# Performance work log

Hardware: AMD Instinct MI355X
Metric: run time of the kernel (lower is better)

Reference implementation:

```python
import jax, jax.numpy as jnp
import numpy as np

N, D = 512, 64          # n_objects, object_dim
HG, OG = 256, 256       # g hidden, g output
HF, OF = 256, 64        # f hidden, f output


def setup_inputs() -> dict:
    key = jax.random.key(0)
    ks = jax.random.split(key, 16)
    s = 0.05
    inp = {
        "x": jax.random.normal(ks[0], (N, D), dtype=jnp.float32),
        "q": jax.random.normal(ks[1], (D,), dtype=jnp.float32),
        # MLP g: input 3*D -> HG -> OG (ReLU after every layer, nonlinear=True)
        "g_w1": jax.random.normal(ks[2], (3 * D, HG), dtype=jnp.float32) * s,
        "g_b1": jnp.zeros((HG,), dtype=jnp.float32),
        "g_w2": jax.random.normal(ks[3], (HG, OG), dtype=jnp.float32) * s,
        "g_b2": jnp.zeros((OG,), dtype=jnp.float32),
        # query_expand: D -> HG -> OG (nonlinear=True)
        "qe_w1": jax.random.normal(ks[4], (D, HG), dtype=jnp.float32) * s,
        "qe_b1": jnp.zeros((HG,), dtype=jnp.float32),
        "qe_w2": jax.random.normal(ks[5], (HG, OG), dtype=jnp.float32) * s,
        "qe_b2": jnp.zeros((OG,), dtype=jnp.float32),
        # MLP f: OG -> HF -> OF (ReLU on hidden only, nonlinear=False)
        "f_w1": jax.random.normal(ks[6], (OG, HF), dtype=jnp.float32) * s,
        "f_b1": jnp.zeros((HF,), dtype=jnp.float32),
        "f_w2": jax.random.normal(ks[7], (HF, OF), dtype=jnp.float32) * s,
        "f_b2": jnp.zeros((OF,), dtype=jnp.float32),
    }
    return inp


def reference(x, q, g_w1, g_b1, g_w2, g_b2, qe_w1, qe_b1, qe_w2, qe_b2,
              f_w1, f_b1, f_w2, f_b2):
    n, d = x.shape
    # pair (a,b): first half x_i = x[b], second half x_j = x[a], then query q
    xi = jnp.broadcast_to(x[None, :, :], (n, n, d))   # repeats x along dim 0
    xj = jnp.broadcast_to(x[:, None, :], (n, n, d))   # repeats x along dim 1
    qb = jnp.broadcast_to(q[None, None, :], (n, n, d))
    pair_concat = jnp.concatenate([xi, xj, qb], axis=-1).reshape(n * n, 3 * d)
    # g MLP (ReLU after every layer since nonlinear=True)
    h = jax.nn.relu(pair_concat @ g_w1 + g_b1)
    relations = jax.nn.relu(h @ g_w2 + g_b2)          # [N*N, OG]
    # attentional weighting
    qh = jax.nn.relu(q @ qe_w1 + qe_b1)
    q_exp = jax.nn.relu(qh @ qe_w2 + qe_b2)           # [OG]
    c = jax.nn.softmax(relations @ q_exp, axis=0)     # [N*N]
    embedding = jnp.sum(relations * c[:, None], axis=0)  # [OG]
    # f MLP (no final nonlinearity)
    fh = jax.nn.relu(embedding @ f_w1 + f_b1)
    out = fh @ f_w2 + f_b2                            # [OF]
    return out
```

## Files before the change

### kernel.cpp

```cpp
#include <hip/hip_runtime.h>
#include <hip/hip_bf16.h>

typedef __attribute__((ext_vector_type(8))) short s16x8;
typedef __attribute__((ext_vector_type(4))) float f32x4;

#define NSLOT 128

__device__ __forceinline__ short f2bf(float f) {
    union { float f; unsigned u; } c; c.f = f;
    unsigned u = c.u;
    return (short)((u + 0x7fffu + ((u >> 16) & 1u)) >> 16);
}
__device__ __forceinline__ float bf2f(short s) {
    union { unsigned u; float f; } c;
    c.u = ((unsigned)(unsigned short)s) << 16;
    return c.f;
}
__device__ __forceinline__ unsigned pk2(float lo, float hi) {
    __hip_bfloat162 p = __float22bfloat162_rn(make_float2(lo, hi));
    return *reinterpret_cast<unsigned*>(&p);
}

#define GLD16(gp, lp) __builtin_amdgcn_global_load_lds( \
    (const __attribute__((address_space(1))) unsigned int*)(gp), \
    (__attribute__((address_space(3))) unsigned int*)(lp), 16, 0, 0)

__global__ __launch_bounds__(256) void rn_k1(
    const float* __restrict__ x, const float* __restrict__ q,
    const float* __restrict__ g_w1, const float* __restrict__ g_b1,
    const float* __restrict__ g_w2,
    const float* __restrict__ qe_w1, const float* __restrict__ qe_b1,
    const float* __restrict__ qe_w2, const float* __restrict__ qe_b2,
    short* __restrict__ u8, float* __restrict__ V,
    float* __restrict__ c0, float* __restrict__ qexp,
    short* __restrict__ w2s, float* __restrict__ accb)
{
    __shared__ float sbuf[64];
    __shared__ float qh[256];
    const int blk = blockIdx.x, t = threadIdx.x;

    if (blk < 512) {
        if (t < 64) sbuf[t] = x[blk * 64 + t];
        __syncthreads();
        float u = 0.f, v = 0.f;
        #pragma unroll 4
        for (int k = 0; k < 64; ++k) {
            float xv = sbuf[k];
            u += xv * g_w1[k * 256 + t];
            v += xv * g_w1[(64 + k) * 256 + t];
        }
        u8[blk * 256 + (t ^ ((blk & 7) << 3))] = f2bf(u);
        V[blk * 256 + t] = v;
        {
            int E = blk * 256 + t;
            int e = E & 7, f = E >> 3;
            int lane = f & 63, n = (f >> 6) & 3, kk = (f >> 8) & 7, wv = (f >> 11) & 3;
            int l15 = lane & 15, g = lane >> 4;
            int col = wv * 64 + n * 16 + l15;
            int k = kk * 32 + g * 8 + e;
            w2s[E] = f2bf(g_w2[k * 256 + col]);
        }
    } else if (blk == 512) {
        if (t < 64) sbuf[t] = q[t];
        __syncthreads();
        float cc = g_b1[t], hh = qe_b1[t];
        #pragma unroll 4
        for (int k = 0; k < 64; ++k) {
            float qv = sbuf[k];
            cc += qv * g_w1[(128 + k) * 256 + t];
            hh += qv * qe_w1[k * 256 + t];
        }
        c0[t] = cc;
        qh[t] = fmaxf(hh, 0.f);
        __syncthreads();
        float qe = qe_b2[t];
        #pragma unroll 4
        for (int k = 0; k < 256; ++k) qe += qh[k] * qe_w2[k * 256 + t];
        qexp[t] = fmaxf(qe, 0.f);
    } else {
        const int total = NSLOT * 257;
        int off = (blk - 513) * 2048 + t * 8;
        #pragma unroll
        for (int i = 0; i < 8; ++i)
            if (off + i < total) accb[off + i] = 0.f;
    }
}

__global__ __launch_bounds__(256, 4) void rn_k2(
    const float* __restrict__ V, const float* __restrict__ c0,
    const float* __restrict__ qexp, const short* __restrict__ u8,
    const short* __restrict__ w2s, const float* __restrict__ g_b2,
    float* __restrict__ accb)
{
    __shared__ short hT[64 * 256];
    __shared__ float srowT[64][4];

    const int bid = blockIdx.x;
    const int a   = bid >> 3;
    const int b0  = (bid & 7) << 6;
    const int tid = threadIdx.x;
    const int wave = tid >> 6, lane = tid & 63;
    const int l15 = lane & 15, g = lane >> 4;
    const int col0 = wave << 6;

    {
        const short* src = u8 + b0 * 256;
        #pragma unroll
        for (int i = 0; i < 8; ++i) {
            const int j = wave * 8 + i;
            GLD16(src + j * 512 + lane * 8, hT + j * 512);
        }
    }

    const int rowb = tid >> 5;
    const int colb = ((tid & 31) * 8) ^ (rowb << 3);
    float vc8[8];
    {
        const float4 vA = *(const float4*)&V[a * 256 + colb];
        const float4 vB = *(const float4*)&V[a * 256 + colb + 4];
        const float4 cA = *(const float4*)&c0[colb];
        const float4 cB = *(const float4*)&c0[colb + 4];
        vc8[0] = vA.x + cA.x; vc8[1] = vA.y + cA.y;
        vc8[2] = vA.z + cA.z; vc8[3] = vA.w + cA.w;
        vc8[4] = vB.x + cB.x; vc8[5] = vB.y + cB.y;
        vc8[6] = vB.z + cB.z; vc8[7] = vB.w + cB.w;
    }

    float qe[4], b2c[4];
    #pragma unroll
    for (int n = 0; n < 4; ++n) {
        int col = col0 + n * 16 + l15;
        qe[n]  = qexp[col];
        b2c[n] = g_b2[col];
    }

    __syncthreads();

    #pragma unroll
    for (int it = 0; it < 8; ++it) {
        const int si = tid * 8 + it * 2048;
        s16x8 raw = *(const s16x8*)&hT[si];
        float h0 = fmaxf(bf2f(raw[0]) + vc8[0], 0.f);
        float h1 = fmaxf(bf2f(raw[1]) + vc8[1], 0.f);
        float h2 = fmaxf(bf2f(raw[2]) + vc8[2], 0.f);
        float h3 = fmaxf(bf2f(raw[3]) + vc8[3], 0.f);
        float h4 = fmaxf(bf2f(raw[4]) + vc8[4], 0.f);
        float h5 = fmaxf(bf2f(raw[5]) + vc8[5], 0.f);
        float h6 = fmaxf(bf2f(raw[6]) + vc8[6], 0.f);
        float h7 = fmaxf(bf2f(raw[7]) + vc8[7], 0.f);
        uint4 ov;
        ov.x = pk2(h0, h1); ov.y = pk2(h2, h3);
        ov.z = pk2(h4, h5); ov.w = pk2(h6, h7);
        *reinterpret_cast<uint4*>(&hT[si]) = ov;
    }
    __syncthreads();

    const short* w2w = w2s + (wave << 14);
#define BFR_LOAD(kk, n) (*(const s16x8*)&w2w[(((kk) * 4 + (n)) << 9) + (lane << 3)])
    const int axor  = (l15 & 7) << 3;
    const int arow0 = l15 * 256;

    f32x4 acc[4][4];
    #pragma unroll
    for (int m = 0; m < 4; ++m)
        #pragma unroll
        for (int n = 0; n < 4; ++n)
            acc[m][n] = (f32x4){0.f, 0.f, 0.f, 0.f};

    #pragma unroll
    for (int kk = 0; kk < 8; ++kk) {
        const int koff = kk * 32 + g * 8;
        s16x8 bfr[4];
        #pragma unroll
        for (int n = 0; n < 4; ++n) bfr[n] = BFR_LOAD(kk, n);
        s16x8 afr[4];
        #pragma unroll
        for (int m = 0; m < 4; ++m)
            afr[m] = *(const s16x8*)&hT[arow0 + m * 4096 + (koff ^ axor)];
        __builtin_amdgcn_s_setprio(1);
        #pragma unroll
        for (int m = 0; m < 4; ++m)
            #pragma unroll
            for (int n = 0; n < 4; ++n)
                acc[m][n] = __builtin_amdgcn_mfma_f32_16x16x32_bf16(
                    afr[m], bfr[n], acc[m][n], 0, 0, 0);
        __builtin_amdgcn_s_setprio(0);
    }
#undef BFR_LOAD

    #pragma unroll
    for (int m = 0; m < 4; ++m)
        #pragma unroll
        for (int n = 0; n < 4; ++n)
            #pragma unroll
            for (int j = 0; j < 4; ++j)
                acc[m][n][j] = fmaxf(acc[m][n][j] + b2c[n], 0.f);

    #pragma unroll
    for (int m = 0; m < 4; ++m) {
        #pragma unroll
        for (int j = 0; j < 4; ++j) {
            float sp = 0.f;
            #pragma unroll
            for (int n = 0; n < 4; ++n) sp += acc[m][n][j] * qe[n];
            sp += __shfl_xor(sp, 1);
            sp += __shfl_xor(sp, 2);
            sp += __shfl_xor(sp, 4);
            sp += __shfl_xor(sp, 8);
            if (l15 == 0) srowT[m * 16 + g * 4 + j][wave] = sp;
        }
    }
    __syncthreads();

    float wrow[4][4];
    #pragma unroll
    for (int m = 0; m < 4; ++m)
        #pragma unroll
        for (int j = 0; j < 4; ++j) {
            const float4 s4 = *(const float4*)&srowT[m * 16 + g * 4 + j][0];
            wrow[m][j] = __expf(s4.x + s4.y + s4.z + s4.w);
        }

    const int slot = bid & (NSLOT - 1);
    if (wave == 0) {
        float ls = 0.f;
        #pragma unroll
        for (int m = 0; m < 4; ++m)
            #pragma unroll
            for (int j = 0; j < 4; ++j) ls += wrow[m][j];
        ls += __shfl_xor(ls, 16);
        ls += __shfl_xor(ls, 32);
        if (lane == 0) atomicAdd(&accb[slot * 257 + 256], ls);
    }

    #pragma unroll
    for (int n = 0; n < 4; ++n) {
        float wv = 0.f;
        #pragma unroll
        for (int m = 0; m < 4; ++m)
            #pragma unroll
            for (int j = 0; j < 4; ++j)
                wv += wrow[m][j] * acc[m][n][j];
        wv += __shfl_xor(wv, 16);
        wv += __shfl_xor(wv, 32);
        if (lane < 16) atomicAdd(&accb[slot * 257 + col0 + n * 16 + lane], wv);
    }
}

__global__ __launch_bounds__(256) void rn_k4(
    const float* __restrict__ accb,
    const float* __restrict__ f_w1, const float* __restrict__ f_b1,
    const float* __restrict__ f_w2, const float* __restrict__ f_b2,
    float* __restrict__ out)
{
    __shared__ float emb[256];
    __shared__ float fh[256];
    const int t = threadIdx.x;

    float v0 = 0.f, v1 = 0.f, v2 = 0.f, v3 = 0.f;
    float ls = 0.f;
    #pragma unroll
    for (int s = 0; s < NSLOT; s += 4) {
        v0 += accb[(s + 0) * 257 + t];
        v1 += accb[(s + 1) * 257 + t];
        v2 += accb[(s + 2) * 257 + t];
        v3 += accb[(s + 3) * 257 + t];
        ls += accb[s * 257 + 256] + accb[(s + 1) * 257 + 256]
            + accb[(s + 2) * 257 + 256] + accb[(s + 3) * 257 + 256];
    }
    emb[t] = (v0 + v1 + v2 + v3) / ls;
    __syncthreads();

    float h0 = f_b1[t], h1 = 0.f, h2 = 0.f, h3 = 0.f;
    #pragma unroll 8
    for (int k = 0; k < 256; k += 4) {
        h0 += emb[k + 0] * f_w1[(k + 0) * 256 + t];
        h1 += emb[k + 1] * f_w1[(k + 1) * 256 + t];
        h2 += emb[k + 2] * f_w1[(k + 2) * 256 + t];
        h3 += emb[k + 3] * f_w1[(k + 3) * 256 + t];
    }
    fh[t] = fmaxf((h0 + h1) + (h2 + h3), 0.f);
    __syncthreads();

    if (t < 64) {
        float o0 = f_b2[t], o1 = 0.f, o2 = 0.f, o3 = 0.f;
        #pragma unroll 8
        for (int k = 0; k < 256; k += 4) {
            o0 += fh[k + 0] * f_w2[(k + 0) * 64 + t];
            o1 += fh[k + 1] * f_w2[(k + 1) * 64 + t];
            o2 += fh[k + 2] * f_w2[(k + 2) * 64 + t];
            o3 += fh[k + 3] * f_w2[(k + 3) * 64 + t];
        }
        out[t] = (o0 + o1) + (o2 + o3);
    }
}

extern "C" void kernel_launch(void* const* d_in, const int* in_sizes, int n_in,
                              void* d_out, int out_size, void* d_ws, size_t ws_size,
                              hipStream_t stream) {
    const float* x     = (const float*)d_in[0];
    const float* q     = (const float*)d_in[1];
    const float* g_w1  = (const float*)d_in[2];
    const float* g_b1  = (const float*)d_in[3];
    const float* g_w2  = (const float*)d_in[4];
    const float* g_b2  = (const float*)d_in[5];
    const float* qe_w1 = (const float*)d_in[6];
    const float* qe_b1 = (const float*)d_in[7];
    const float* qe_w2 = (const float*)d_in[8];
    const float* qe_b2 = (const float*)d_in[9];
    const float* f_w1  = (const float*)d_in[10];
    const float* f_b1  = (const float*)d_in[11];
    const float* f_w2  = (const float*)d_in[12];
    const float* f_b2  = (const float*)d_in[13];

    float* wsf  = (float*)d_ws;
    short* u8   = (short*)wsf;
    float* V    = wsf + 65536;
    float* c0   = wsf + 196608;
    float* qexp = wsf + 196864;
    short* w2s  = (short*)(wsf + 197120);
    float* accb = wsf + 229888;

    hipLaunchKernelGGL(rn_k1, dim3(530), dim3(256), 0, stream,
                       x, q, g_w1, g_b1, g_w2, qe_w1, qe_b1, qe_w2, qe_b2,
                       u8, V, c0, qexp, w2s, accb);
    hipLaunchKernelGGL(rn_k2, dim3(4096), dim3(256), 0, stream,
                       V, c0, qexp, (const short*)u8, (const short*)w2s, g_b2, accb);
    hipLaunchKernelGGL(rn_k4, dim3(1), dim3(256), 0, stream,
                       accb, f_w1, f_b1, f_w2, f_b2, (float*)d_out);
}
```

Baseline: 72.10 us.

## Persist rn_k2 blocks over four tiles with async prefetch, parallelize final MLP

The main kernel now launches a quarter as many blocks, and each block loops over four (a, b0) tiles. It issues global-to-LDS loads for the next tile's u8 rows and V vector while it does the softmax and atomic accumulation for the current tile, so load latency overlaps with work and per-block setup (qe, b2, c0 loads) is amortized. The finishing kernel uses 1024 threads and splits the slot reduction and both f-MLP matvecs across four k-slices. Risks: the four tiles in each block run serially, the occupancy hint drops to 3, and fewer blocks means less parallelism to hide latency.

```diff
diff --git a/kernel.cpp b/kernel.cpp
--- a/kernel.cpp
+++ b/kernel.cpp
@@ -86,45 +86,20 @@
     }
 }
 
-__global__ __launch_bounds__(256, 4) void rn_k2(
+__global__ __launch_bounds__(256, 3) void rn_k2(
     const float* __restrict__ V, const float* __restrict__ c0,
     const float* __restrict__ qexp, const short* __restrict__ u8,
     const short* __restrict__ w2s, const float* __restrict__ g_b2,
     float* __restrict__ accb)
 {
-    __shared__ short hT[64 * 256];
+    __shared__ short hT[16384];
     __shared__ float srowT[64][4];
 
     const int bid = blockIdx.x;
-    const int a   = bid >> 3;
-    const int b0  = (bid & 7) << 6;
     const int tid = threadIdx.x;
     const int wave = tid >> 6, lane = tid & 63;
     const int l15 = lane & 15, g = lane >> 4;
     const int col0 = wave << 6;
-
-    {
-        const short* src = u8 + b0 * 256;
-        #pragma unroll
-        for (int i = 0; i < 8; ++i) {
-            const int j = wave * 8 + i;
-            GLD16(src + j * 512 + lane * 8, hT + j * 512);
-        }
-    }
-
-    const int rowb = tid >> 5;
-    const int colb = ((tid & 31) * 8) ^ (rowb << 3);
-    float vc8[8];
-    {
-        const float4 vA = *(const float4*)&V[a * 256 + colb];
-        const float4 vB = *(const float4*)&V[a * 256 + colb + 4];
-        const float4 cA = *(const float4*)&c0[colb];
-        const float4 cB = *(const float4*)&c0[colb + 4];
-        vc8[0] = vA.x + cA.x; vc8[1] = vA.y + cA.y;
-        vc8[2] = vA.z + cA.z; vc8[3] = vA.w + cA.w;
-        vc8[4] = vB.x + cB.x; vc8[5] = vB.y + cB.y;
-        vc8[6] = vB.z + cB.z; vc8[7] = vB.w + cB.w;
-    }
 
     float qe[4], b2c[4];
     #pragma unroll
@@ -133,166 +108,223 @@
         qe[n]  = qexp[col];
         b2c[n] = g_b2[col];
     }
-
-    __syncthreads();
-
-    #pragma unroll
-    for (int it = 0; it < 8; ++it) {
-        const int si = tid * 8 + it * 2048;
-        s16x8 raw = *(const s16x8*)&hT[si];
-        float h0 = fmaxf(bf2f(raw[0]) + vc8[0], 0.f);
-        float h1 = fmaxf(bf2f(raw[1]) + vc8[1], 0.f);
-        float h2 = fmaxf(bf2f(raw[2]) + vc8[2], 0.f);
-        float h3 = fmaxf(bf2f(raw[3]) + vc8[3], 0.f);
-        float h4 = fmaxf(bf2f(raw[4]) + vc8[4], 0.f);
-        float h5 = fmaxf(bf2f(raw[5]) + vc8[5], 0.f);
-        float h6 = fmaxf(bf2f(raw[6]) + vc8[6], 0.f);
-        float h7 = fmaxf(bf2f(raw[7]) + vc8[7], 0.f);
-        uint4 ov;
-        ov.x = pk2(h0, h1); ov.y = pk2(h2, h3);
-        ov.z = pk2(h4, h5); ov.w = pk2(h6, h7);
-        *reinterpret_cast<uint4*>(&hT[si]) = ov;
-    }
-    __syncthreads();
-
+    const int rowb = tid >> 5;
+    const int colb = ((tid & 31) * 8) ^ (rowb << 3);
+    float c8[8];
+    {
+        const float4 cA = *(const float4*)&c0[colb];
+        const float4 cB = *(const float4*)&c0[colb + 4];
+        c8[0] = cA.x; c8[1] = cA.y; c8[2] = cA.z; c8[3] = cA.w;
+        c8[4] = cB.x; c8[5] = cB.y; c8[6] = cB.z; c8[7] = cB.w;
+    }
     const short* w2w = w2s + (wave << 14);
-#define BFR_LOAD(kk, n) (*(const s16x8*)&w2w[(((kk) * 4 + (n)) << 9) + (lane << 3)])
     const int axor  = (l15 & 7) << 3;
     const int arow0 = l15 * 256;
 
-    f32x4 acc[4][4];
-    #pragma unroll
-    for (int m = 0; m < 4; ++m)
-        #pragma unroll
-        for (int n = 0; n < 4; ++n)
-            acc[m][n] = (f32x4){0.f, 0.f, 0.f, 0.f};
-
-    #pragma unroll
-    for (int kk = 0; kk < 8; ++kk) {
-        const int koff = kk * 32 + g * 8;
-        s16x8 bfr[4];
-        #pragma unroll
-        for (int n = 0; n < 4; ++n) bfr[n] = BFR_LOAD(kk, n);
-        s16x8 afr[4];
+    float vc8[8];
+    {
+        const int v0 = bid << 2;
+        const short* src = u8 + ((v0 & 7) << 6) * 256;
+        #pragma unroll
+        for (int i = 0; i < 8; ++i) {
+            const int seg = wave + (i << 2);
+            GLD16(src + seg * 512 + lane * 8, hT + seg * 512);
+        }
+        const int a0 = v0 >> 3;
+        const float4 vA = *(const float4*)&V[a0 * 256 + colb];
+        const float4 vB = *(const float4*)&V[a0 * 256 + colb + 4];
+        vc8[0] = vA.x + c8[0]; vc8[1] = vA.y + c8[1];
+        vc8[2] = vA.z + c8[2]; vc8[3] = vA.w + c8[3];
+        vc8[4] = vB.x + c8[4]; vc8[5] = vB.y + c8[5];
+        vc8[6] = vB.z + c8[6]; vc8[7] = vB.w + c8[7];
+    }
+
+    for (int k = 0; k < 4; ++k) {
+        const int vv = (bid << 2) + k;
+        const int slot = vv & (NSLOT - 1);
+
+        asm volatile("s_waitcnt vmcnt(0)" ::: "memory");
+        __builtin_amdgcn_sched_barrier(0);
+
+        #pragma unroll
+        for (int it = 0; it < 8; ++it) {
+            const int si = tid * 8 + it * 2048;
+            s16x8 raw = *(const s16x8*)&hT[si];
+            float h0 = fmaxf(bf2f(raw[0]) + vc8[0], 0.f);
+            float h1 = fmaxf(bf2f(raw[1]) + vc8[1], 0.f);
+            float h2 = fmaxf(bf2f(raw[2]) + vc8[2], 0.f);
+            float h3 = fmaxf(bf2f(raw[3]) + vc8[3], 0.f);
+            float h4 = fmaxf(bf2f(raw[4]) + vc8[4], 0.f);
+            float h5 = fmaxf(bf2f(raw[5]) + vc8[5], 0.f);
+            float h6 = fmaxf(bf2f(raw[6]) + vc8[6], 0.f);
+            float h7 = fmaxf(bf2f(raw[7]) + vc8[7], 0.f);
+            uint4 ov;
+            ov.x = pk2(h0, h1); ov.y = pk2(h2, h3);
+            ov.z = pk2(h4, h5); ov.w = pk2(h6, h7);
+            *reinterpret_cast<uint4*>(&hT[si]) = ov;
+        }
+        __syncthreads();
+
+#define BFR_LOAD(kk, n) (*(const s16x8*)&w2w[(((kk) * 4 + (n)) << 9) + (lane << 3)])
+        f32x4 acc[4][4];
         #pragma unroll
         for (int m = 0; m < 4; ++m)
-            afr[m] = *(const s16x8*)&hT[arow0 + m * 4096 + (koff ^ axor)];
-        __builtin_amdgcn_s_setprio(1);
+            #pragma unroll
+            for (int n = 0; n < 4; ++n)
+                acc[m][n] = (f32x4){0.f, 0.f, 0.f, 0.f};
+
+        #pragma unroll
+        for (int kk = 0; kk < 8; ++kk) {
+            const int koff = kk * 32 + g * 8;
+            s16x8 bfr[4];
+            #pragma unroll
+            for (int n = 0; n < 4; ++n) bfr[n] = BFR_LOAD(kk, n);
+            s16x8 afr[4];
+            #pragma unroll
+            for (int m = 0; m < 4; ++m)
+                afr[m] = *(const s16x8*)&hT[arow0 + m * 4096 + (koff ^ axor)];
+            __builtin_amdgcn_s_setprio(1);
+            #pragma unroll
+            for (int m = 0; m < 4; ++m)
+                #pragma unroll
+                for (int n = 0; n < 4; ++n)
+                    acc[m][n] = __builtin_amdgcn_mfma_f32_16x16x32_bf16(
+                        afr[m], bfr[n], acc[m][n], 0, 0, 0);
+            __builtin_amdgcn_s_setprio(0);
+        }
+#undef BFR_LOAD
+
         #pragma unroll
         for (int m = 0; m < 4; ++m)
             #pragma unroll
             for (int n = 0; n < 4; ++n)
-                acc[m][n] = __builtin_amdgcn_mfma_f32_16x16x32_bf16(
-                    afr[m], bfr[n], acc[m][n], 0, 0, 0);
-        __builtin_amdgcn_s_setprio(0);
-    }
-#undef BFR_LOAD
-
-    #pragma unroll
-    for (int m = 0; m < 4; ++m)
-        #pragma unroll
-        for (int n = 0; n < 4; ++n)
-            #pragma unroll
-            for (int j = 0; j < 4; ++j)
-                acc[m][n][j] = fmaxf(acc[m][n][j] + b2c[n], 0.f);
-
-    #pragma unroll
-    for (int m = 0; m < 4; ++m) {
-        #pragma unroll
-        for (int j = 0; j < 4; ++j) {
-            float sp = 0.f;
-            #pragma unroll
-            for (int n = 0; n < 4; ++n) sp += acc[m][n][j] * qe[n];
-            sp += __shfl_xor(sp, 1);
-            sp += __shfl_xor(sp, 2);
-            sp += __shfl_xor(sp, 4);
-            sp += __shfl_xor(sp, 8);
-            if (l15 == 0) srowT[m * 16 + g * 4 + j][wave] = sp;
-        }
-    }
-    __syncthreads();
-
-    float wrow[4][4];
-    #pragma unroll
-    for (int m = 0; m < 4; ++m)
-        #pragma unroll
-        for (int j = 0; j < 4; ++j) {
-            const float4 s4 = *(const float4*)&srowT[m * 16 + g * 4 + j][0];
-            wrow[m][j] = __expf(s4.x + s4.y + s4.z + s4.w);
-        }
-
-    const int slot = bid & (NSLOT - 1);
-    if (wave == 0) {
-        float ls = 0.f;
+                #pragma unroll
+                for (int j = 0; j < 4; ++j)
+                    acc[m][n][j] = fmaxf(acc[m][n][j] + b2c[n], 0.f);
+
+        #pragma unroll
+        for (int m = 0; m < 4; ++m) {
+            #pragma unroll
+            for (int j = 0; j < 4; ++j) {
+                float sp = 0.f;
+                #pragma unroll
+                for (int n = 0; n < 4; ++n) sp += acc[m][n][j] * qe[n];
+                sp += __shfl_xor(sp, 1);
+                sp += __shfl_xor(sp, 2);
+                sp += __shfl_xor(sp, 4);
+                sp += __shfl_xor(sp, 8);
+                if (l15 == 0) srowT[m * 16 + g * 4 + j][wave] = sp;
+            }
+        }
+        __syncthreads();
+
+        if (k < 3) {
+            const int vn = vv + 1;
+            const short* srcn = u8 + ((vn & 7) << 6) * 256;
+            #pragma unroll
+            for (int i = 0; i < 8; ++i) {
+                const int seg = wave + (i << 2);
+                GLD16(srcn + seg * 512 + lane * 8, hT + seg * 512);
+            }
+            const int an = vn >> 3;
+            const float4 vA = *(const float4*)&V[an * 256 + colb];
+            const float4 vB = *(const float4*)&V[an * 256 + colb + 4];
+            vc8[0] = vA.x + c8[0]; vc8[1] = vA.y + c8[1];
+            vc8[2] = vA.z + c8[2]; vc8[3] = vA.w + c8[3];
+            vc8[4] = vB.x + c8[4]; vc8[5] = vB.y + c8[5];
+            vc8[6] = vB.z + c8[6]; vc8[7] = vB.w + c8[7];
+        }
+
+        float wrow[4][4];
         #pragma unroll
         for (int m = 0; m < 4; ++m)
             #pragma unroll
-            for (int j = 0; j < 4; ++j) ls += wrow[m][j];
-        ls += __shfl_xor(ls, 16);
-        ls += __shfl_xor(ls, 32);
-        if (lane == 0) atomicAdd(&accb[slot * 257 + 256], ls);
-    }
-
-    #pragma unroll
-    for (int n = 0; n < 4; ++n) {
-        float wv = 0.f;
-        #pragma unroll
-        for (int m = 0; m < 4; ++m)
-            #pragma unroll
-            for (int j = 0; j < 4; ++j)
-                wv += wrow[m][j] * acc[m][n][j];
-        wv += __shfl_xor(wv, 16);
-        wv += __shfl_xor(wv, 32);
-        if (lane < 16) atomicAdd(&accb[slot * 257 + col0 + n * 16 + lane], wv);
-    }
-}
-
-__global__ __launch_bounds__(256) void rn_k4(
+            for (int j = 0; j < 4; ++j) {
+                const float4 s4 = *(const float4*)&srowT[m * 16 + g * 4 + j][0];
+                wrow[m][j] = __expf(s4.x + s4.y + s4.z + s4.w);
+            }
+
+        if (wave == 0) {
+            float ls = 0.f;
+            #pragma unroll
+            for (int m = 0; m < 4; ++m)
+                #pragma unroll
+                for (int j = 0; j < 4; ++j) ls += wrow[m][j];
+            ls += __shfl_xor(ls, 16);
+            ls += __shfl_xor(ls, 32);
+            if (lane == 0) atomicAdd(&accb[slot * 257 + 256], ls);
+        }
+
+        #pragma unroll
+        for (int n = 0; n < 4; ++n) {
+            float wv = 0.f;
+            #pragma unroll
+            for (int m = 0; m < 4; ++m)
+                #pragma unroll
+                for (int j = 0; j < 4; ++j)
+                    wv += wrow[m][j] * acc[m][n][j];
+            wv += __shfl_xor(wv, 16);
+            wv += __shfl_xor(wv, 32);
+            if (lane < 16) atomicAdd(&accb[slot * 257 + col0 + n * 16 + lane], wv);
+        }
+    }
+}
+
+__global__ __launch_bounds__(1024) void rn_k4(
     const float* __restrict__ accb,
     const float* __restrict__ f_w1, const float* __restrict__ f_b1,
     const float* __restrict__ f_w2, const float* __restrict__ f_b2,
     float* __restrict__ out)
 {
+    __shared__ float part[4][256];
     __shared__ float emb[256];
     __shared__ float fh[256];
-    const int t = threadIdx.x;
-
-    float v0 = 0.f, v1 = 0.f, v2 = 0.f, v3 = 0.f;
-    float ls = 0.f;
-    #pragma unroll
-    for (int s = 0; s < NSLOT; s += 4) {
-        v0 += accb[(s + 0) * 257 + t];
-        v1 += accb[(s + 1) * 257 + t];
-        v2 += accb[(s + 2) * 257 + t];
-        v3 += accb[(s + 3) * 257 + t];
-        ls += accb[s * 257 + 256] + accb[(s + 1) * 257 + 256]
-            + accb[(s + 2) * 257 + 256] + accb[(s + 3) * 257 + 256];
-    }
-    emb[t] = (v0 + v1 + v2 + v3) / ls;
-    __syncthreads();
-
-    float h0 = f_b1[t], h1 = 0.f, h2 = 0.f, h3 = 0.f;
+    __shared__ float lsa[128];
+    const int t   = threadIdx.x;
+    const int col = t & 255;
+    const int sl  = t >> 8;
+
+    float v = 0.f;
     #pragma unroll 8
-    for (int k = 0; k < 256; k += 4) {
-        h0 += emb[k + 0] * f_w1[(k + 0) * 256 + t];
-        h1 += emb[k + 1] * f_w1[(k + 1) * 256 + t];
-        h2 += emb[k + 2] * f_w1[(k + 2) * 256 + t];
-        h3 += emb[k + 3] * f_w1[(k + 3) * 256 + t];
-    }
-    fh[t] = fmaxf((h0 + h1) + (h2 + h3), 0.f);
-    __syncthreads();
-
-    if (t < 64) {
-        float o0 = f_b2[t], o1 = 0.f, o2 = 0.f, o3 = 0.f;
+    for (int s = sl; s < NSLOT; s += 4) v += accb[s * 257 + col];
+    part[sl][col] = v;
+    if (t < 128) lsa[t] = accb[t * 257 + 256];
+    __syncthreads();
+
+    if (sl == 0) {
+        float ls = 0.f;
         #pragma unroll 8
-        for (int k = 0; k < 256; k += 4) {
-            o0 += fh[k + 0] * f_w2[(k + 0) * 64 + t];
-            o1 += fh[k + 1] * f_w2[(k + 1) * 64 + t];
-            o2 += fh[k + 2] * f_w2[(k + 2) * 64 + t];
-            o3 += fh[k + 3] * f_w2[(k + 3) * 64 + t];
-        }
-        out[t] = (o0 + o1) + (o2 + o3);
-    }
+        for (int s = 0; s < 128; ++s) ls += lsa[s];
+        emb[col] = (part[0][col] + part[1][col] + part[2][col] + part[3][col]) / ls;
+    }
+    __syncthreads();
+
+    {
+        float h = 0.f;
+        const int k0 = sl << 6;
+        #pragma unroll 8
+        for (int k = 0; k < 64; ++k)
+            h += emb[k0 + k] * f_w1[(k0 + k) * 256 + col];
+        part[sl][col] = h;
+    }
+    __syncthreads();
+    if (sl == 0)
+        fh[col] = fmaxf(part[0][col] + part[1][col] + part[2][col] + part[3][col]
+                        + f_b1[col], 0.f);
+    __syncthreads();
+
+    if (t < 256) {
+        const int oc = t & 63, ks = t >> 6;
+        float o = 0.f;
+        const int k0 = ks << 6;
+        #pragma unroll 8
+        for (int k = 0; k < 64; ++k)
+            o += fh[k0 + k] * f_w2[(k0 + k) * 64 + oc];
+        part[ks][oc] = o;
+    }
+    __syncthreads();
+    if (t < 64)
+        out[t] = part[0][t] + part[1][t] + part[2][t] + part[3][t] + f_b2[t];
 }
 
 extern "C" void kernel_launch(void* const* d_in, const int* in_sizes, int n_in,
@@ -324,8 +356,8 @@
     hipLaunchKernelGGL(rn_k1, dim3(530), dim3(256), 0, stream,
                        x, q, g_w1, g_b1, g_w2, qe_w1, qe_b1, qe_w2, qe_b2,
                        u8, V, c0, qexp, w2s, accb);
-    hipLaunchKernelGGL(rn_k2, dim3(4096), dim3(256), 0, stream,
+    hipLaunchKernelGGL(rn_k2, dim3(1024), dim3(256), 0, stream,
                        V, c0, qexp, (const short*)u8, (const short*)w2s, g_b2, accb);
-    hipLaunchKernelGGL(rn_k4, dim3(1), dim3(256), 0, stream,
+    hipLaunchKernelGGL(rn_k4, dim3(1), dim3(1024), 0, stream,
                        accb, f_w1, f_b1, f_w2, f_b2, (float*)d_out);
 }
```

After: 174.1 us. 2.41x slower.
